# Kernel tuning notes

Hardware: AMD Instinct MI355X
Metric: run time of the kernel (lower is better)

Reference implementation:

```python
import jax, jax.numpy as jnp
import numpy as np

B, S, NU, ML, H, V = 32, 256, 4, 9, 768, 30522


def setup_inputs() -> dict:
    key = jax.random.key(0)
    ks = jax.random.split(key, 13)
    s = 1.0 / np.sqrt(H)
    return {
        "x": jax.random.randint(ks[0], (B, S), 0, V),
        "decoder_input": jax.random.normal(ks[1], (B, NU, H), jnp.float32) * 0.02,
        "encoder_output": jax.random.normal(ks[2], (B, S, H), jnp.float32) * 0.02,
        "hidden": jax.random.normal(ks[3], (1, B, H), jnp.float32) * 0.02,
        "max_len": ML,
        "teacher": jax.random.randint(ks[4], (B, NU, ML), 0, V),
        "embed_w": jax.random.normal(ks[5], (V, H), jnp.float32) * 0.02,
        "gru_w_ih": jax.random.uniform(ks[6], (3 * H, H), jnp.float32, -s, s),
        "gru_w_hh": jax.random.uniform(ks[7], (3 * H, H), jnp.float32, -s, s),
        "gru_b_ih": jax.random.uniform(ks[8], (3 * H,), jnp.float32, -s, s),
        "gru_b_hh": jax.random.uniform(ks[9], (3 * H,), jnp.float32, -s, s),
        "w_gen_w": jax.random.uniform(ks[10], (1, 3 * H), jnp.float32, -s, s),
        "w_gen_b": jax.random.uniform(ks[11], (1,), jnp.float32, -s, s),
    }


def reference(x, decoder_input, encoder_output, hidden, max_len, teacher,
              embed_w, gru_w_ih, gru_w_hh, gru_b_ih, gru_b_hh, w_gen_w, w_gen_b):
    pad_mask = (x == 0)                       # [B, S]
    b, nu, h_dim = decoder_input.shape
    h0 = hidden[0]                            # [B, H]

    # Teacher-forced input sequence for every (update, step): [NU*ML, B, H]
    tf = embed_w[teacher[:, :, :max_len - 1]]           # [B, NU, ML-1, H]
    tf = jnp.moveaxis(tf, 0, 2)                          # [NU, ML-1, B, H]
    first = jnp.swapaxes(decoder_input, 0, 1)[:, None]   # [NU, 1, B, H]
    ws = jnp.concatenate([first, tf], axis=1).reshape(nu * max_len, b, h_dim)

    def gru_cell(w, h):
        gi = w @ gru_w_ih.T + gru_b_ih        # [B, 3H]
        gh = h @ gru_w_hh.T + gru_b_hh
        i_r, i_z, i_n = jnp.split(gi, 3, axis=-1)
        h_r, h_z, h_n = jnp.split(gh, 3, axis=-1)
        r = jax.nn.sigmoid(i_r + h_r)
        z = jax.nn.sigmoid(i_z + h_z)
        n = jnp.tanh(i_n + r * h_n)
        return (1.0 - z) * n + z * h

    batch_idx = jnp.arange(b)[:, None]

    def step(h, w):
        h = gru_cell(w, h)                                    # [B, H]
        attn_e = jnp.einsum('bsh,bh->bs', encoder_output, h)  # [B, S]
        attn_e = jnp.where(pad_mask, -1e9, attn_e)
        attn_history = jax.nn.softmax(attn_e, axis=-1)        # [B, S]
        attn_vocab = jax.nn.softmax(h @ embed_w.T, axis=-1)   # [B, V]
        context = jnp.einsum('bs,bsh->bh', attn_history, encoder_output)
        gate_in = jnp.concatenate([w, h, context], axis=-1)   # [B, 3H]
        p_gen = jax.nn.sigmoid(gate_in @ w_gen_w.T + w_gen_b) # [B, 1]
        p_ctx = jnp.zeros_like(attn_vocab).at[batch_idx, x].add(attn_history)
        p_final = p_gen * attn_vocab + (1.0 - p_gen) * p_ctx  # [B, V]
        return h, p_final

    _, outs = jax.lax.scan(step, h0, ws)          # [NU*ML, B, V]
    outs = outs.reshape(nu, max_len, b, -1)       # [NU, ML, B, V]
    return jnp.transpose(outs, (2, 0, 1, 3))      # [B, NU, ML, V]
```

## Files before the change

### kernel.cpp

```cpp
#include <hip/hip_runtime.h>
#include <math.h>

#define BB_ 32
#define SS_ 256
#define HH_ 768
#define VV_ 30522
#define TT_ 36
#define MM_ 1152
#define NBLK_GRU 48

typedef __bf16 bf16x8 __attribute__((ext_vector_type(8)));
typedef __bf16 bf16x4 __attribute__((ext_vector_type(4)));
typedef float f32x4 __attribute__((ext_vector_type(4)));
typedef unsigned int u32x4 __attribute__((ext_vector_type(4)));

__device__ __forceinline__ float sigmoidf_(float x) { return 1.f / (1.f + expf(-x)); }

__device__ __forceinline__ void async_load16(const void* g, void* l) {
  __builtin_amdgcn_global_load_lds(
      (const __attribute__((address_space(1))) void*)g,
      (__attribute__((address_space(3))) void*)l, 16, 0, 0);
}

__global__ __launch_bounds__(256) void cvt_bf16(const float* __restrict__ s,
                                                __bf16* __restrict__ d, int n4) {
  int i = blockIdx.x * 256 + threadIdx.x;
  if (i < n4) {
    float4 v = reinterpret_cast<const float4*>(s)[i];
    bf16x4 o;
    o[0] = (__bf16)v.x; o[1] = (__bf16)v.y; o[2] = (__bf16)v.z; o[3] = (__bf16)v.w;
    reinterpret_cast<bf16x4*>(d)[i] = o;
  }
}

__global__ __launch_bounds__(256) void build_ws(const float* __restrict__ dec,
                                                const int* __restrict__ teacher,
                                                const float* __restrict__ embed,
                                                __bf16* __restrict__ wsbf) {
  int idx = blockIdx.x * 256 + threadIdx.x;
  if (idx >= MM_ * HH_) return;
  int m = idx / HH_, k = idx - m * HH_;
  int tau = m >> 5, b = m & 31;
  int u = tau / 9, tt = tau - u * 9;
  float v;
  if (tt == 0) v = dec[((size_t)b * 4 + u) * HH_ + k];
  else v = embed[(size_t)teacher[(b * 4 + u) * 9 + tt - 1] * HH_ + k];
  wsbf[idx] = (__bf16)v;
}

__global__ __launch_bounds__(256) void enc_gate(const float* __restrict__ enc,
                                                const float* __restrict__ wgen,
                                                float* __restrict__ encg) {
  int row = blockIdx.x * 4 + (threadIdx.x >> 6);
  int lane = threadIdx.x & 63;
  const float* er = enc + (size_t)row * HH_;
  float ssum = 0.f;
#pragma unroll
  for (int i = 0; i < 12; ++i) ssum += er[i * 64 + lane] * wgen[1536 + i * 64 + lane];
  for (int off = 32; off; off >>= 1) ssum += __shfl_down(ssum, off);
  if (lane == 0) encg[row] = ssum;
}

template <int MODE>
__global__ __launch_bounds__(256) void gemm_bt2(const __bf16* __restrict__ A,
                                                const __bf16* __restrict__ Bm,
                                                float* __restrict__ C,
                                                float* __restrict__ rowsum,
                                                int Nreal, int ldC) {
  __shared__ __bf16 As[128 * 32];
  __shared__ __bf16 Bs[128 * 32];
  const int tid = threadIdx.x;
  const int lane = tid & 63, wave = tid >> 6;
  const int wm = wave >> 1, wn = wave & 1;
  const int q = lane >> 4, ln = lane & 15;
  const int m0 = blockIdx.y * 128, n0 = blockIdx.x * 128;
  const int srow = (wave << 5) + (lane >> 2);
  const int kc = lane & 3;
  const size_t aoff = (size_t)(m0 + srow) * HH_ + kc * 8;
  const size_t aoff2 = aoff + 16 * HH_;
  int br1 = n0 + srow;      if (br1 >= Nreal) br1 = Nreal - 1;
  int br2 = n0 + srow + 16; if (br2 >= Nreal) br2 = Nreal - 1;
  __bf16* lA1 = &As[srow * 32 + kc * 8];
  __bf16* lA2 = &As[(srow + 16) * 32 + kc * 8];
  __bf16* lB1 = &Bs[srow * 32 + kc * 8];
  __bf16* lB2 = &Bs[(srow + 16) * 32 + kc * 8];
  f32x4 acc[4][4] = {};
  for (int kb = 0; kb < 24; ++kb) {
    const int k0 = kb << 5;
    async_load16(A + aoff + k0, lA1);
    async_load16(A + aoff2 + k0, lA2);
    async_load16(Bm + (size_t)br1 * HH_ + kc * 8 + k0, lB1);
    async_load16(Bm + (size_t)br2 * HH_ + kc * 8 + k0, lB2);
    __syncthreads();
    bf16x8 af[4], bfr[4];
#pragma unroll
    for (int mi = 0; mi < 4; ++mi)
      af[mi] = *reinterpret_cast<const bf16x8*>(&As[(wm * 64 + mi * 16 + ln) * 32 + q * 8]);
#pragma unroll
    for (int ni = 0; ni < 4; ++ni)
      bfr[ni] = *reinterpret_cast<const bf16x8*>(&Bs[(wn * 64 + ni * 16 + ln) * 32 + q * 8]);
#pragma unroll
    for (int mi = 0; mi < 4; ++mi)
#pragma unroll
      for (int ni = 0; ni < 4; ++ni)
        acc[mi][ni] = __builtin_amdgcn_mfma_f32_16x16x32_bf16(af[mi], bfr[ni], acc[mi][ni], 0, 0, 0);
    __syncthreads();
  }
#pragma unroll
  for (int mi = 0; mi < 4; ++mi)
#pragma unroll
    for (int r2 = 0; r2 < 4; ++r2) {
      const int m = m0 + wm * 64 + mi * 16 + q * 4 + r2;
      if (MODE == 0) {
#pragma unroll
        for (int ni = 0; ni < 4; ++ni) {
          int n = n0 + wn * 64 + ni * 16 + ln;
          if (n < Nreal) C[(size_t)m * ldC + n] = acc[mi][ni][r2];
        }
      } else {
        float part = 0.f;
#pragma unroll
        for (int ni = 0; ni < 4; ++ni) {
          int n = n0 + wn * 64 + ni * 16 + ln;
          float e = expf(fminf(acc[mi][ni][r2], 60.f));
          if (n < Nreal) { C[(size_t)m * ldC + n] = e; part += e; }
        }
#pragma unroll
        for (int o = 1; o < 16; o <<= 1) part += __shfl_xor(part, o);
        if (ln == 0) atomicAdd(rowsum + m, part);
      }
    }
}

__global__ __launch_bounds__(128, 1) void gru_scan(const __bf16* __restrict__ hid_bf,
                                                   const float* __restrict__ H0,
                                                   const __bf16* __restrict__ Whh,
                                                   const float* __restrict__ GI,
                                                   const float* __restrict__ bih,
                                                   const float* __restrict__ bhh,
                                                   __bf16* __restrict__ Ah,
                                                   __bf16* __restrict__ Hx,
                                                   unsigned* __restrict__ flags) {
  __shared__ __bf16 WhhS[48 * HH_];
  const int tid = threadIdx.x, lane = tid & 63;
  const int mi = tid >> 6;
  const int q = lane >> 4, ln = lane & 15;
  const int jH = blockIdx.x * 16 + ln;
  for (int i = tid; i < 48 * 96; i += 128) {
    int row = i / 96, cs = i - row * 96;
    int g = row >> 4, jl = row & 15;
    bf16x8 v = *reinterpret_cast<const bf16x8*>(
        &Whh[((size_t)(g * 768 + blockIdx.x * 16 + jl)) * HH_ + cs * 8]);
    *reinterpret_cast<bf16x8*>(&WhhS[row * HH_ + ((cs ^ (row & 7)) * 8)]) = v;
  }
  const float bir = bih[jH], biz = bih[jH + 768], bin_ = bih[jH + 1536];
  const float bhr = bhh[jH], bhz = bhh[jH + 768], bhn = bhh[jH + 1536];
  float hc[4];
#pragma unroll
  for (int r2 = 0; r2 < 4; ++r2)
    hc[r2] = H0[(size_t)(mi * 16 + q * 4 + r2) * HH_ + jH];
  const __bf16* w0 = &WhhS[(0 + ln) * HH_];
  const __bf16* w1 = &WhhS[(16 + ln) * HH_];
  const __bf16* w2 = &WhhS[(32 + ln) * HH_];
  const int swz = (ln & 7) * 8;
  float gir[4], giz[4], gin[4];
#pragma unroll
  for (int r2 = 0; r2 < 4; ++r2) {
    const float* gi = GI + (size_t)(mi * 16 + q * 4 + r2) * 2304;
    gir[r2] = gi[jH]; giz[r2] = gi[jH + 768]; gin[r2] = gi[jH + 1536];
  }
  __syncthreads();
  for (int tau = 0; tau < TT_; ++tau) {
    const __bf16* arow = tau ? (Hx + (size_t)(((tau - 1) & 1) * 32 + mi * 16 + ln) * HH_)
                             : (hid_bf + (size_t)(mi * 16 + ln) * HH_);
    u32x4 raw[24];
#pragma unroll
    for (int kb = 0; kb < 24; ++kb) {
      const __bf16* ap = arow + kb * 32 + q * 8;
      asm volatile("global_load_dwordx4 %0, %1, off sc1"
                   : "=v"(raw[kb]) : "v"(ap) : "memory");
    }
    asm volatile("s_waitcnt vmcnt(0)" ::: "memory");
    __builtin_amdgcn_sched_barrier(0);
    f32x4 a0 = {}, a1 = {}, a2 = {};
#pragma unroll
    for (int kb = 0; kb < 24; ++kb) {
      bf16x8 a = __builtin_bit_cast(bf16x8, raw[kb]);
      int kl = (kb * 32 + q * 8) ^ swz;
      bf16x8 b0 = *reinterpret_cast<const bf16x8*>(w0 + kl);
      bf16x8 b1 = *reinterpret_cast<const bf16x8*>(w1 + kl);
      bf16x8 b2 = *reinterpret_cast<const bf16x8*>(w2 + kl);
      a0 = __builtin_amdgcn_mfma_f32_16x16x32_bf16(a, b0, a0, 0, 0, 0);
      a1 = __builtin_amdgcn_mfma_f32_16x16x32_bf16(a, b1, a1, 0, 0, 0);
      a2 = __builtin_amdgcn_mfma_f32_16x16x32_bf16(a, b2, a2, 0, 0, 0);
    }
    __bf16* hxc = Hx + (size_t)((tau & 1) * 32) * HH_;
#pragma unroll
    for (int r2 = 0; r2 < 4; ++r2) {
      int b = mi * 16 + q * 4 + r2;
      float r = sigmoidf_(gir[r2] + bir + a0[r2] + bhr);
      float z = sigmoidf_(giz[r2] + biz + a1[r2] + bhz);
      float n = tanhf(gin[r2] + bin_ + r * (a2[r2] + bhn));
      float h = (1.f - z) * n + z * hc[r2];
      hc[r2] = h;
      float hp = __shfl_xor(h, 1);
      __bf16 hb = (__bf16)h, hpb = (__bf16)hp;
      unsigned lo = (unsigned)__builtin_bit_cast(unsigned short, hb);
      unsigned hi = (unsigned)__builtin_bit_cast(unsigned short, hpb);
      if (!(ln & 1)) {
        unsigned u = lo | (hi << 16);
        *reinterpret_cast<unsigned*>(&Ah[((size_t)b * TT_ + tau) * HH_ + jH]) = u;
        if (tau < TT_ - 1)
          __hip_atomic_store(reinterpret_cast<unsigned*>(&hxc[(size_t)b * HH_ + jH]), u,
                             __ATOMIC_RELAXED, __HIP_MEMORY_SCOPE_AGENT);
      }
    }
    if (tau < TT_ - 1) {
      asm volatile("s_waitcnt vmcnt(0)" ::: "memory");
      if (lane == 0)
        __hip_atomic_store(&flags[(size_t)(blockIdx.x * 2 + mi) * 16], (unsigned)(tau + 1),
                           __ATOMIC_RELAXED, __HIP_MEMORY_SCOPE_AGENT);
      {
        const float* GIt = GI + (size_t)(tau + 1) * BB_ * 2304;
#pragma unroll
        for (int r2 = 0; r2 < 4; ++r2) {
          const float* gi = GIt + (size_t)(mi * 16 + q * 4 + r2) * 2304;
          gir[r2] = gi[jH]; giz[r2] = gi[jH + 768]; gin[r2] = gi[jH + 1536];
        }
      }
      const unsigned tgt = (unsigned)(tau + 1);
      int ok = 0, spin = 0;
      while (!ok) {
        unsigned v = (lane < NBLK_GRU)
            ? __hip_atomic_load(&flags[(size_t)(lane * 2 + mi) * 16], __ATOMIC_RELAXED,
                                __HIP_MEMORY_SCOPE_AGENT)
            : tgt;
        ok = __all((int)(v >= tgt));
        if (!ok) {
          __builtin_amdgcn_s_sleep(1);
          if (++spin > (1 << 20)) break;
        }
      }
    }
  }
}

__global__ __launch_bounds__(256) void attn_gemm(const __bf16* __restrict__ Ah,
                                                 const __bf16* __restrict__ encb,
                                                 float* __restrict__ E) {
  int b = blockIdx.x >> 2, stile = blockIdx.x & 3;
  int wave = threadIdx.x >> 6, lane = threadIdx.x & 63;
  int q = lane >> 4, ln = lane & 15;
  int s = stile * 64 + wave * 16 + ln;
  const __bf16* brow = encb + ((size_t)b * SS_ + s) * HH_;
  const __bf16* arow[3];
#pragma unroll
  for (int mt = 0; mt < 3; ++mt) {
    int tau = mt * 16 + ln; if (tau > 35) tau = 35;
    arow[mt] = Ah + ((size_t)b * TT_ + tau) * HH_;
  }
  f32x4 acc[3] = {};
#pragma unroll 4
  for (int kb = 0; kb < 24; ++kb) {
    int k0 = kb * 32 + q * 8;
    bf16x8 bb = *reinterpret_cast<const bf16x8*>(brow + k0);
#pragma unroll
    for (int mt = 0; mt < 3; ++mt) {
      bf16x8 aa = *reinterpret_cast<const bf16x8*>(arow[mt] + k0);
      acc[mt] = __builtin_amdgcn_mfma_f32_16x16x32_bf16(aa, bb, acc[mt], 0, 0, 0);
    }
  }
#pragma unroll
  for (int mt = 0; mt < 3; ++mt)
#pragma unroll
    for (int r2 = 0; r2 < 4; ++r2) {
      int tau = mt * 16 + q * 4 + r2;
      if (tau < 36) E[((size_t)b * TT_ + tau) * SS_ + s] = acc[mt][r2];
    }
}

__global__ __launch_bounds__(256) void softmax_pg(const float* __restrict__ E,
                                                  const int* __restrict__ x,
                                                  const float* __restrict__ encg,
                                                  const __bf16* __restrict__ wsbf,
                                                  const __bf16* __restrict__ Ah,
                                                  const float* __restrict__ wgen,
                                                  const float* __restrict__ wgenb,
                                                  float* __restrict__ attn,
                                                  float* __restrict__ pg) {
  int m = blockIdx.x;
  int b = m / TT_, tau = m - b * TT_;
  int m_in = tau * 32 + b;
  int t = threadIdx.x;
  __shared__ float red[256];
  __shared__ float r1[256], r2[256], r3[256];
  float e = E[(size_t)m * SS_ + t];
  if (x[b * SS_ + t] == 0) e = -1000000000.0f;
  red[t] = e; __syncthreads();
  for (int off = 128; off; off >>= 1) {
    if (t < off) red[t] = fmaxf(red[t], red[t + off]);
    __syncthreads();
  }
  float mx = red[0];
  float p = expf(e - mx);
  float dsum = 0.f;
#pragma unroll
  for (int i = 0; i < 3; ++i) {
    int k = t + i * 256;
    dsum += (float)wsbf[(size_t)m_in * HH_ + k] * wgen[k];
    dsum += (float)Ah[(size_t)m * HH_ + k] * wgen[768 + k];
  }
  float pe = p * encg[b * SS_ + t];
  r1[t] = p; r2[t] = pe; r3[t] = dsum; __syncthreads();
  for (int off = 128; off; off >>= 1) {
    if (t < off) { r1[t] += r1[t + off]; r2[t] += r2[t + off]; r3[t] += r3[t + off]; }
    __syncthreads();
  }
  float Z = r1[0];
  attn[(size_t)m * SS_ + t] = p / Z;
  if (t == 0) pg[m] = sigmoidf_(r3[0] + r2[0] / Z + wgenb[0]);
}

__global__ __launch_bounds__(256) void finalize(float* __restrict__ C,
                                                const float* __restrict__ rowsum,
                                                const float* __restrict__ pg) {
  int m = blockIdx.y;
  float scale = pg[m] / rowsum[m];
  int base_i = blockIdx.x * 2048;
  size_t rowb = (size_t)m * VV_;
#pragma unroll
  for (int j = 0; j < 8; ++j) {
    int i = base_i + j * 256 + threadIdx.x;
    if (i < VV_) C[rowb + i] *= scale;
  }
}

__global__ __launch_bounds__(256) void scatter_ctx(float* __restrict__ C,
                                                   const float* __restrict__ attn,
                                                   const float* __restrict__ pg,
                                                   const int* __restrict__ x) {
  int m = blockIdx.x, s = threadIdx.x;
  int b = m / TT_;
  float v = (1.f - pg[m]) * attn[(size_t)m * SS_ + s];
  int col = x[b * SS_ + s];
  atomicAdd(C + (size_t)m * VV_ + col, v);
}

extern "C" void kernel_launch(void* const* d_in, const int* in_sizes, int n_in,
                              void* d_out, int out_size, void* d_ws, size_t ws_size,
                              hipStream_t stream) {
  const int*   x       = (const int*)d_in[0];
  const float* dec     = (const float*)d_in[1];
  const float* enc     = (const float*)d_in[2];
  const float* hidden  = (const float*)d_in[3];
  const int*   teacher = (const int*)d_in[5];
  const float* embed   = (const float*)d_in[6];
  const float* wih     = (const float*)d_in[7];
  const float* whh     = (const float*)d_in[8];
  const float* bih     = (const float*)d_in[9];
  const float* bhh     = (const float*)d_in[10];
  const float* wgen    = (const float*)d_in[11];
  const float* wgenb   = (const float*)d_in[12];
  float* out = (float*)d_out;

  char* w = (char*)d_ws;
  __bf16* embed_bf = (__bf16*)w;  w += (size_t)VV_ * HH_ * 2;
  __bf16* enc_bf   = (__bf16*)w;  w += (size_t)BB_ * SS_ * HH_ * 2;
  __bf16* wih_bf   = (__bf16*)w;  w += (size_t)2304 * HH_ * 2;
  __bf16* whh_bf   = (__bf16*)w;  w += (size_t)2304 * HH_ * 2;
  __bf16* ws_bf    = (__bf16*)w;  w += (size_t)MM_ * HH_ * 2;
  __bf16* hid_bf   = (__bf16*)w;  w += (size_t)BB_ * HH_ * 2;
  __bf16* A_h      = (__bf16*)w;  w += (size_t)MM_ * HH_ * 2;
  float*  GI       = (float*)w;   w += (size_t)MM_ * 2304 * 4;
  float*  E        = (float*)w;   w += (size_t)MM_ * SS_ * 4;
  float*  attn     = (float*)w;   w += (size_t)MM_ * SS_ * 4;
  float*  encg     = (float*)w;   w += (size_t)BB_ * SS_ * 4;
  float*  pg       = (float*)w;   w += 8192;
  char*   ctl      = w;           w += 16384;
  __bf16* Hx       = (__bf16*)w;  w += (size_t)2 * BB_ * HH_ * 2;
  float*    rowsum = (float*)ctl;
  unsigned* flags  = (unsigned*)(ctl + 4864);

  hipMemsetAsync(ctl, 0, 16384, stream);

  cvt_bf16<<<(VV_ * HH_ / 4 + 255) / 256, 256, 0, stream>>>(embed, embed_bf, VV_ * HH_ / 4);
  cvt_bf16<<<(BB_ * SS_ * HH_ / 4 + 255) / 256, 256, 0, stream>>>(enc, enc_bf, BB_ * SS_ * HH_ / 4);
  cvt_bf16<<<(2304 * HH_ / 4 + 255) / 256, 256, 0, stream>>>(wih, wih_bf, 2304 * HH_ / 4);
  cvt_bf16<<<(2304 * HH_ / 4 + 255) / 256, 256, 0, stream>>>(whh, whh_bf, 2304 * HH_ / 4);
  cvt_bf16<<<(BB_ * HH_ / 4 + 255) / 256, 256, 0, stream>>>(hidden, hid_bf, BB_ * HH_ / 4);

  build_ws<<<(MM_ * HH_ + 255) / 256, 256, 0, stream>>>(dec, teacher, embed, ws_bf);

  gemm_bt2<0><<<dim3(2304 / 128, MM_ / 128), 256, 0, stream>>>(ws_bf, wih_bf, GI, nullptr, 2304, 2304);

  enc_gate<<<BB_ * SS_ / 4, 256, 0, stream>>>(enc, wgen, encg);

  gru_scan<<<NBLK_GRU, 128, 0, stream>>>(hid_bf, hidden, whh_bf, GI, bih, bhh, A_h, Hx, flags);

  attn_gemm<<<BB_ * 4, 256, 0, stream>>>(A_h, enc_bf, E);
  softmax_pg<<<MM_, 256, 0, stream>>>(E, x, encg, ws_bf, A_h, wgen, wgenb, attn, pg);

  gemm_bt2<1><<<dim3((VV_ + 127) / 128, MM_ / 128), 256, 0, stream>>>(A_h, embed_bf, out, rowsum, VV_, VV_);

  finalize<<<dim3((VV_ + 2047) / 2048, MM_), 256, 0, stream>>>(out, rowsum, pg);
  scatter_ctx<<<MM_, 256, 0, stream>>>(out, attn, pg, x);
}
```

Before: 763.5 us.

## Fuse vocab softmax normalization into GEMM via grid-wide per-row-block barrier

The vocab GEMM now keeps exp'd logits in registers, accumulates row sums atomically, then waits on a per-row-block completion counter until all 239 column tiles finish before writing normalized, p_gen-scaled values. This removes the separate finalize pass that re-read and re-wrote the full output, which is large. It relies on all 239x9 blocks being co-resident. Otherwise the spin-wait can only end through the iteration cap, which would give wrong or slow results. Block occupancy and register pressure from holding the accumulators across the wait are further risks.

```diff
diff --git a/kernel.cpp b/kernel.cpp
--- a/kernel.cpp
+++ b/kernel.cpp
@@ -8,6 +8,7 @@
 #define TT_ 36
 #define MM_ 1152
 #define NBLK_GRU 48
+#define NTILE_V 239
 
 typedef __bf16 bf16x8 __attribute__((ext_vector_type(8)));
 typedef __bf16 bf16x4 __attribute__((ext_vector_type(4)));
@@ -61,12 +62,9 @@
   if (lane == 0) encg[row] = ssum;
 }
 
-template <int MODE>
 __global__ __launch_bounds__(256) void gemm_bt2(const __bf16* __restrict__ A,
                                                 const __bf16* __restrict__ Bm,
-                                                float* __restrict__ C,
-                                                float* __restrict__ rowsum,
-                                                int Nreal, int ldC) {
+                                                float* __restrict__ C) {
   __shared__ __bf16 As[128 * 32];
   __shared__ __bf16 Bs[128 * 32];
   const int tid = threadIdx.x;
@@ -78,8 +76,64 @@
   const int kc = lane & 3;
   const size_t aoff = (size_t)(m0 + srow) * HH_ + kc * 8;
   const size_t aoff2 = aoff + 16 * HH_;
-  int br1 = n0 + srow;      if (br1 >= Nreal) br1 = Nreal - 1;
-  int br2 = n0 + srow + 16; if (br2 >= Nreal) br2 = Nreal - 1;
+  __bf16* lA1 = &As[srow * 32 + kc * 8];
+  __bf16* lA2 = &As[(srow + 16) * 32 + kc * 8];
+  __bf16* lB1 = &Bs[srow * 32 + kc * 8];
+  __bf16* lB2 = &Bs[(srow + 16) * 32 + kc * 8];
+  f32x4 acc[4][4] = {};
+  for (int kb = 0; kb < 24; ++kb) {
+    const int k0 = kb << 5;
+    async_load16(A + aoff + k0, lA1);
+    async_load16(A + aoff2 + k0, lA2);
+    async_load16(Bm + (size_t)(n0 + srow) * HH_ + kc * 8 + k0, lB1);
+    async_load16(Bm + (size_t)(n0 + srow + 16) * HH_ + kc * 8 + k0, lB2);
+    __syncthreads();
+    bf16x8 af[4], bfr[4];
+#pragma unroll
+    for (int mi = 0; mi < 4; ++mi)
+      af[mi] = *reinterpret_cast<const bf16x8*>(&As[(wm * 64 + mi * 16 + ln) * 32 + q * 8]);
+#pragma unroll
+    for (int ni = 0; ni < 4; ++ni)
+      bfr[ni] = *reinterpret_cast<const bf16x8*>(&Bs[(wn * 64 + ni * 16 + ln) * 32 + q * 8]);
+#pragma unroll
+    for (int mi = 0; mi < 4; ++mi)
+#pragma unroll
+      for (int ni = 0; ni < 4; ++ni)
+        acc[mi][ni] = __builtin_amdgcn_mfma_f32_16x16x32_bf16(af[mi], bfr[ni], acc[mi][ni], 0, 0, 0);
+    __syncthreads();
+  }
+#pragma unroll
+  for (int mi = 0; mi < 4; ++mi)
+#pragma unroll
+    for (int r2 = 0; r2 < 4; ++r2) {
+      const int m = m0 + wm * 64 + mi * 16 + q * 4 + r2;
+#pragma unroll
+      for (int ni = 0; ni < 4; ++ni) {
+        int n = n0 + wn * 64 + ni * 16 + ln;
+        C[(size_t)m * 2304 + n] = acc[mi][ni][r2];
+      }
+    }
+}
+
+__global__ __launch_bounds__(256) void gemm_vocab(const __bf16* __restrict__ A,
+                                                  const __bf16* __restrict__ Bm,
+                                                  float* __restrict__ C,
+                                                  float* __restrict__ rowsum,
+                                                  const float* __restrict__ pg,
+                                                  unsigned* __restrict__ done) {
+  __shared__ __bf16 As[128 * 32];
+  __shared__ __bf16 Bs[128 * 32];
+  const int tid = threadIdx.x;
+  const int lane = tid & 63, wave = tid >> 6;
+  const int wm = wave >> 1, wn = wave & 1;
+  const int q = lane >> 4, ln = lane & 15;
+  const int m0 = blockIdx.y * 128, n0 = blockIdx.x * 128;
+  const int srow = (wave << 5) + (lane >> 2);
+  const int kc = lane & 3;
+  const size_t aoff = (size_t)(m0 + srow) * HH_ + kc * 8;
+  const size_t aoff2 = aoff + 16 * HH_;
+  int br1 = n0 + srow;      if (br1 >= VV_) br1 = VV_ - 1;
+  int br2 = n0 + srow + 16; if (br2 >= VV_) br2 = VV_ - 1;
   __bf16* lA1 = &As[srow * 32 + kc * 8];
   __bf16* lA2 = &As[(srow + 16) * 32 + kc * 8];
   __bf16* lB1 = &Bs[srow * 32 + kc * 8];
@@ -111,23 +165,43 @@
 #pragma unroll
     for (int r2 = 0; r2 < 4; ++r2) {
       const int m = m0 + wm * 64 + mi * 16 + q * 4 + r2;
-      if (MODE == 0) {
-#pragma unroll
-        for (int ni = 0; ni < 4; ++ni) {
-          int n = n0 + wn * 64 + ni * 16 + ln;
-          if (n < Nreal) C[(size_t)m * ldC + n] = acc[mi][ni][r2];
-        }
-      } else {
-        float part = 0.f;
-#pragma unroll
-        for (int ni = 0; ni < 4; ++ni) {
-          int n = n0 + wn * 64 + ni * 16 + ln;
-          float e = expf(fminf(acc[mi][ni][r2], 60.f));
-          if (n < Nreal) { C[(size_t)m * ldC + n] = e; part += e; }
-        }
-#pragma unroll
-        for (int o = 1; o < 16; o <<= 1) part += __shfl_xor(part, o);
-        if (ln == 0) atomicAdd(rowsum + m, part);
+      float part = 0.f;
+#pragma unroll
+      for (int ni = 0; ni < 4; ++ni) {
+        int n = n0 + wn * 64 + ni * 16 + ln;
+        float e = expf(fminf(acc[mi][ni][r2], 60.f));
+        acc[mi][ni][r2] = e;
+        if (n < VV_) part += e;
+      }
+#pragma unroll
+      for (int o = 1; o < 16; o <<= 1) part += __shfl_xor(part, o);
+      if (ln == 0) atomicAdd(rowsum + m, part);
+    }
+  __threadfence();
+  __syncthreads();
+  if (tid == 0)
+    __hip_atomic_fetch_add(&done[(size_t)blockIdx.y * 16], 1u,
+                           __ATOMIC_RELEASE, __HIP_MEMORY_SCOPE_AGENT);
+  if (wave == 0) {
+    int spin = 0;
+    while (__hip_atomic_load(&done[(size_t)blockIdx.y * 16], __ATOMIC_ACQUIRE,
+                             __HIP_MEMORY_SCOPE_AGENT) < (unsigned)NTILE_V) {
+      __builtin_amdgcn_s_sleep(8);
+      if (++spin > (1 << 22)) break;
+    }
+  }
+  __syncthreads();
+#pragma unroll
+  for (int mi = 0; mi < 4; ++mi)
+#pragma unroll
+    for (int r2 = 0; r2 < 4; ++r2) {
+      const int m = m0 + wm * 64 + mi * 16 + q * 4 + r2;
+      float rs = __hip_atomic_load(rowsum + m, __ATOMIC_RELAXED, __HIP_MEMORY_SCOPE_AGENT);
+      float scale = pg[m] / rs;
+#pragma unroll
+      for (int ni = 0; ni < 4; ++ni) {
+        int n = n0 + wn * 64 + ni * 16 + ln;
+        if (n < VV_) C[(size_t)m * VV_ + n] = acc[mi][ni][r2] * scale;
       }
     }
 }
@@ -321,20 +395,6 @@
   if (t == 0) pg[m] = sigmoidf_(r3[0] + r2[0] / Z + wgenb[0]);
 }
 
-__global__ __launch_bounds__(256) void finalize(float* __restrict__ C,
-                                                const float* __restrict__ rowsum,
-                                                const float* __restrict__ pg) {
-  int m = blockIdx.y;
-  float scale = pg[m] / rowsum[m];
-  int base_i = blockIdx.x * 2048;
-  size_t rowb = (size_t)m * VV_;
-#pragma unroll
-  for (int j = 0; j < 8; ++j) {
-    int i = base_i + j * 256 + threadIdx.x;
-    if (i < VV_) C[rowb + i] *= scale;
-  }
-}
-
 __global__ __launch_bounds__(256) void scatter_ctx(float* __restrict__ C,
                                                    const float* __restrict__ attn,
                                                    const float* __restrict__ pg,
@@ -380,6 +440,7 @@
   __bf16* Hx       = (__bf16*)w;  w += (size_t)2 * BB_ * HH_ * 2;
   float*    rowsum = (float*)ctl;
   unsigned* flags  = (unsigned*)(ctl + 4864);
+  unsigned* done   = (unsigned*)(ctl + 4864 + 96 * 64);
 
   hipMemsetAsync(ctl, 0, 16384, stream);
 
@@ -391,7 +452,7 @@
 
   build_ws<<<(MM_ * HH_ + 255) / 256, 256, 0, stream>>>(dec, teacher, embed, ws_bf);
 
-  gemm_bt2<0><<<dim3(2304 / 128, MM_ / 128), 256, 0, stream>>>(ws_bf, wih_bf, GI, nullptr, 2304, 2304);
+  gemm_bt2<<<dim3(2304 / 128, MM_ / 128), 256, 0, stream>>>(ws_bf, wih_bf, GI);
 
   enc_gate<<<BB_ * SS_ / 4, 256, 0, stream>>>(enc, wgen, encg);
 
@@ -400,8 +461,7 @@
   attn_gemm<<<BB_ * 4, 256, 0, stream>>>(A_h, enc_bf, E);
   softmax_pg<<<MM_, 256, 0, stream>>>(E, x, encg, ws_bf, A_h, wgen, wgenb, attn, pg);
 
-  gemm_bt2<1><<<dim3((VV_ + 127) / 128, MM_ / 128), 256, 0, stream>>>(A_h, embed_bf, out, rowsum, VV_, VV_);
-
-  finalize<<<dim3((VV_ + 2047) / 2048, MM_), 256, 0, stream>>>(out, rowsum, pg);
+  gemm_vocab<<<dim3(NTILE_V, MM_ / 128), 256, 0, stream>>>(A_h, embed_bf, out, rowsum, pg, done);
+
   scatter_ctx<<<MM_, 256, 0, stream>>>(out, attn, pg, x);
 }
```

Measured after the change: 1.170 ms. +53.2%, slower.
